# Kernel tuning notes

Hardware: AMD Instinct MI355X
Metric: run time of the kernel (lower is better)

The kernel has to match this reference:

```python
import jax, jax.numpy as jnp
import numpy as np

HIDDEN = 1024
N_HEAD = 16
HEAD_DIM = HIDDEN // N_HEAD


def _rope(x):
    # x: [b, h, l, d]; interleaved RoPE, matching the torch module exactly
    L, d = x.shape[-2], x.shape[-1]
    pos = jnp.arange(L, dtype=x.dtype)[:, None]                      # [L, 1]
    ids = jnp.arange(d // 2, dtype=x.dtype)
    theta = jnp.power(jnp.asarray(10000.0, x.dtype), 2.0 * ids / d)  # [d/2]
    ang = pos / theta                                                # [L, d/2]
    sin = jnp.repeat(jnp.sin(ang), 2, axis=-1)                       # [L, d]
    cos = jnp.repeat(jnp.cos(ang), 2, axis=-1)                       # [L, d]
    # rotate pairs: (x0, x1) -> (-x1, x0)
    x_rot = jnp.stack([-x[..., 1::2], x[..., 0::2]], axis=-1).reshape(x.shape)
    return x * cos + x_rot * sin


def setup_inputs() -> dict:
    key = jax.random.key(0)
    ks = jax.random.split(key, 5)
    B, LQ, LK = 8, 1024, 2048
    scale = 1.0 / np.sqrt(HIDDEN)
    return {
        "x": jax.random.normal(ks[0], (B, LQ, HIDDEN), dtype=jnp.float32),
        "y": jax.random.normal(ks[1], (B, LK, HIDDEN), dtype=jnp.float32),
        "Wq": jax.random.normal(ks[2], (HIDDEN, HIDDEN), dtype=jnp.float32) * scale,
        "Wkv": jax.random.normal(ks[3], (2 * HIDDEN, HIDDEN), dtype=jnp.float32) * scale,
        "Wo": jax.random.normal(ks[4], (HIDDEN, HIDDEN), dtype=jnp.float32) * scale,
    }


def reference(x, y, Wq, Wkv, Wo):
    B, LQ, _ = x.shape
    LK = y.shape[1]
    # projections (torch Linear: out = in @ W.T)
    q = (x @ Wq.T).reshape(B, LQ, N_HEAD, HEAD_DIM).transpose(0, 2, 1, 3)   # [b,h,lq,d]
    kv = (y @ Wkv.T).reshape(B, LK, N_HEAD, 2 * HEAD_DIM).transpose(0, 2, 1, 3)
    k, v = jnp.split(kv, 2, axis=-1)                                         # [b,h,lk,d] each
    q = _rope(q)
    k = _rope(k)
    # NOTE: the original forward does NOT apply self.scale, no dropout, no mask (eval mode)
    scores = jnp.einsum("bhqd,bhkd->bhqk", q, k)
    probs = jax.nn.softmax(scores, axis=-1)
    out = jnp.einsum("bhqk,bhkd->bhqd", probs, v)
    out = out.transpose(0, 2, 1, 3).reshape(B, LQ, HIDDEN)
    return out @ Wo.T
```

## Files before the change

kernel.cpp:

```cpp
#include <hip/hip_runtime.h>

typedef _Float16 f16;
typedef __attribute__((ext_vector_type(8))) _Float16 f16x8;
typedef __attribute__((ext_vector_type(4))) _Float16 f16x4;
typedef __attribute__((ext_vector_type(2))) _Float16 f16x2;
typedef __attribute__((ext_vector_type(4))) float f32x4;

constexpr int B_ = 8, LQ = 1024, LK = 2048, NH = 16, HID = 1024;

__device__ __forceinline__ void gll16(const void* g, void* l) {
  __builtin_amdgcn_global_load_lds((const __attribute__((address_space(1))) void*)g,
                                   (__attribute__((address_space(3))) void*)l, 16, 0, 0);
}

__device__ __forceinline__ f16x2 cvt_pk(float a, float b) {
  return __builtin_bit_cast(f16x2, __builtin_amdgcn_cvt_pkrtz(a, b));
}

constexpr int NQ0 = B_ * LQ * HID / 4;
constexpr int NQ1 = B_ * LK * HID / 4;
constexpr int NQ2 = HID * HID / 4;
constexpr int NQ3 = 2 * HID * HID / 4;
constexpr int NQ4 = HID * HID / 4;
constexpr int NQT = NQ0 + NQ1 + NQ2 + NQ3 + NQ4;

__device__ __forceinline__ void cvt4(const float* __restrict__ s, f16* __restrict__ d, int i) {
  float4 v = ((const float4*)s)[i];
  f16x4 o = {(f16)v.x, (f16)v.y, (f16)v.z, (f16)v.w};
  ((f16x4*)d)[i] = o;
}

__global__ __launch_bounds__(256) void cvt5(const float* __restrict__ x,
                                            const float* __restrict__ y,
                                            const float* __restrict__ wq,
                                            const float* __restrict__ wkv,
                                            const float* __restrict__ wo,
                                            f16* __restrict__ xb, f16* __restrict__ yb,
                                            f16* __restrict__ wqb, f16* __restrict__ wkvb,
                                            f16* __restrict__ wob) {
  int t = blockIdx.x * 256 + threadIdx.x;
  if (t < NQ0) cvt4(x, xb, t);
  else if (t < NQ0 + NQ1) cvt4(y, yb, t - NQ0);
  else if (t < NQ0 + NQ1 + NQ2) cvt4(wq, wqb, t - NQ0 - NQ1);
  else if (t < NQ0 + NQ1 + NQ2 + NQ3) cvt4(wkv, wkvb, t - NQ0 - NQ1 - NQ2);
  else cvt4(wo, wob, t - NQ0 - NQ1 - NQ2 - NQ3);
}

template <int MODE>
__global__ __launch_bounds__(256) void gemm_fused(const f16* __restrict__ A,
                                                  const f16* __restrict__ Bm,
                                                  void* __restrict__ out0,
                                                  void* __restrict__ out1,
                                                  int M, int N, int K) {
  const int gx = gridDim.x;
  const int nwg = gx * gridDim.y;
  const int cpx = nwg >> 3;
  const int fid = blockIdx.y * gx + blockIdx.x;
  const int lid = (fid & 7) * cpx + (fid >> 3);
  const int n0 = (lid % gx) * 128, m0 = (lid / gx) * 128;
  const int tid = threadIdx.x, lane = tid & 63, w = tid >> 6;
  const int wm = w >> 1, wn = w & 1;
  const int quad = lane >> 4, l16 = lane & 15;
  __shared__ __align__(16) f16 As[2][128 * 64];
  __shared__ __align__(16) f16 Bs[2][128 * 64];
  f32x4 acc[4][4] = {};
  const int sr = tid >> 3, sc8 = tid & 7;
  const int ldst = sr * 64 + sc8 * 8;
  const f16* ga = A + (size_t)(m0 + sr) * K + ((sc8 ^ (sr & 7)) << 3);
  const f16* gb = Bm + (size_t)(n0 + sr) * K + ((sc8 ^ (sr & 7)) << 3);
  const int NT = K >> 6;

  auto STAGE = [&](int t) {
    f16* as = As[t & 1];
    f16* bs = Bs[t & 1];
    const int k0 = t << 6;
#pragma unroll
    for (int p = 0; p < 4; ++p) {
      gll16(ga + (size_t)p * 32 * K + k0, &as[ldst + p * 32 * 64]);
      gll16(gb + (size_t)p * 32 * K + k0, &bs[ldst + p * 32 * 64]);
    }
  };

  STAGE(0);
  asm volatile("s_waitcnt vmcnt(0)" ::: "memory");
  __builtin_amdgcn_s_barrier();
  __builtin_amdgcn_sched_barrier(0);

  const int swr = l16 & 7;
  for (int t = 0; t < NT; ++t) {
    if (t + 1 < NT) STAGE(t + 1);
    const f16* as = As[t & 1];
    const f16* bs = Bs[t & 1];
#pragma unroll
    for (int ks = 0; ks < 2; ++ks) {
      f16x8 af[4], bfr[4];
#pragma unroll
      for (int i = 0; i < 4; ++i) {
        const int csw = ((ks * 4 + quad) ^ swr) << 3;
        af[i] = *(const f16x8*)&as[(wm * 64 + i * 16 + l16) * 64 + csw];
        bfr[i] = *(const f16x8*)&bs[(wn * 64 + i * 16 + l16) * 64 + csw];
      }
      __builtin_amdgcn_s_setprio(1);
#pragma unroll
      for (int i = 0; i < 4; ++i)
#pragma unroll
        for (int j = 0; j < 4; ++j)
          acc[i][j] = __builtin_amdgcn_mfma_f32_16x16x32_f16(af[i], bfr[j], acc[i][j], 0, 0, 0);
      __builtin_amdgcn_s_setprio(0);
    }
    asm volatile("s_waitcnt vmcnt(0)" ::: "memory");
    __builtin_amdgcn_s_barrier();
    __builtin_amdgcn_sched_barrier(0);
  }
  if (MODE == 2) {
#pragma unroll
    for (int i = 0; i < 4; ++i)
#pragma unroll
      for (int j = 0; j < 4; ++j) {
        int row = m0 + wm * 64 + i * 16 + quad * 4;
        int col = n0 + wn * 64 + j * 16 + l16;
#pragma unroll
        for (int r = 0; r < 4; ++r)
          ((float*)out0)[(size_t)(row + r) * N + col] = acc[i][j][r];
      }
    return;
  }
  constexpr int LSH = (MODE == 0) ? 10 : 11;
  constexpr int LMSK = (MODE == 0) ? 1023 : 2047;
  const int Ltok = LMSK + 1;
  constexpr float QSCALE = (MODE == 0) ? 1.44269504f : 1.0f;
  if (MODE == 0 || wn == 0) {
#pragma unroll
    for (int j = 0; j < 4; ++j) {
      int c = n0 + wn * 64 + j * 16 + l16;
      int h = (MODE == 0) ? (c >> 6) : (n0 >> 7);
      int d = (MODE == 0) ? (c & 63) : (j * 16 + l16);
      float inv_t = exp2f((float)(d >> 1) * -0.41524101186091903f);
#pragma unroll
      for (int i = 0; i < 4; ++i) {
        f32x4 v = acc[i][j];
        f32x4 pv;
#pragma unroll
        for (int r = 0; r < 4; ++r) pv[r] = __shfl_xor(v[r], 1, 64);
        int row0 = m0 + wm * 64 + i * 16 + quad * 4;
#pragma unroll
        for (int r = 0; r < 4; ++r) {
          int row = row0 + r;
          int pos = row & LMSK, b = row >> LSH;
          float ang = (float)pos * inv_t;
          float sn, cs;
          __sincosf(ang, &sn, &cs);
          float o = (d & 1) ? (v[r] * cs + pv[r] * sn) : (v[r] * cs - pv[r] * sn);
          int dsw = (MODE == 1) ? (d ^ ((pos & 7) << 3)) : d;
          ((f16*)out0)[(((size_t)b * NH + h) * Ltok + pos) * 64 + dsw] = (f16)(o * QSCALE);
        }
      }
    }
  } else {
    const int h = n0 >> 7;
#pragma unroll
    for (int j = 0; j < 4; ++j) {
      int dv = j * 16 + l16;
#pragma unroll
      for (int i = 0; i < 4; ++i) {
        int row0 = m0 + wm * 64 + i * 16 + quad * 4;
        int pos0 = row0 & 2047, b = row0 >> 11;
        int kc = pos0 >> 6, klo = pos0 & 63;
        f32x4 v = acc[i][j];
        f16x4 pk = {(f16)v[0], (f16)v[1], (f16)v[2], (f16)v[3]};
        int klosw = klo ^ ((dv & 7) << 3);
        *(f16x4*)&((f16*)out1)[((((size_t)b * NH + h) * 32 + kc) * 64 + dv) * 64 + klosw] = pk;
      }
    }
  }
}

__global__ __launch_bounds__(256, 4) void attn(const f16* __restrict__ Qb,
                                               const f16* __restrict__ Kb,
                                               const f16* __restrict__ Vt,
                                               f16* __restrict__ attnb) {
  const int fid = blockIdx.x;
  const int lid = (fid & 7) * 128 + (fid >> 3);
  const int bh = lid >> 3, b = bh >> 4, h = bh & 15;
  const int q0 = (lid & 7) * 128;
  const int tid = threadIdx.x, lane = tid & 63, w = tid >> 6;
  const int quad = lane >> 4, l16 = lane & 15;
  const int sw = (l16 & 7) << 3;
  __shared__ __align__(16) f16 Ks[2][64 * 64];
  __shared__ __align__(16) f16 Vts[2][64 * 64];
  const f16* qptr = Qb + ((size_t)bh * LQ + q0 + 32 * w + l16) * 64;
  f16x8 qf[2][2];
#pragma unroll
  for (int qs = 0; qs < 2; ++qs) {
    qf[qs][0] = *(const f16x8*)&qptr[qs * 16 * 64 + quad * 8];
    qf[qs][1] = *(const f16x8*)&qptr[qs * 16 * 64 + 32 + quad * 8];
  }
  const f16x4 ones4 = {(f16)1.f, (f16)1.f, (f16)1.f, (f16)1.f};
  f32x4 o[2][4] = {};
  f32x4 lacc[2] = {};
  float m_run[2] = {0.0f, 0.0f};
  const f16* kbase = Kb + (size_t)bh * LK * 64;
  const f16* vtb = Vt + (size_t)bh * 32 * 4096;
  const int sr = tid >> 3, sc = (tid & 7) * 8;

  auto STAGE = [&](int c) {
    f16* ks = Ks[c & 1];
    f16* vs = Vts[c & 1];
    gll16(kbase + (size_t)(c * 64 + sr) * 64 + sc, &ks[sr * 64 + sc]);
    gll16(kbase + (size_t)(c * 64 + sr + 32) * 64 + sc, &ks[(sr + 32) * 64 + sc]);
    gll16(vtb + (size_t)(c * 64 + sr) * 64 + sc, &vs[sr * 64 + sc]);
    gll16(vtb + (size_t)(c * 64 + sr + 32) * 64 + sc, &vs[(sr + 32) * 64 + sc]);
  };

  constexpr int NC = LK / 64;
  STAGE(0);
  asm volatile("s_waitcnt vmcnt(0)" ::: "memory");
  __builtin_amdgcn_s_barrier();
  __builtin_amdgcn_sched_barrier(0);

  for (int c = 0; c < NC; ++c) {
    if (c + 1 < NC) STAGE(c + 1);
    const f16* Ksb = Ks[c & 1];
    const f16* Vsb = Vts[c & 1];
    f32x4 minit[2];
#pragma unroll
    for (int qs = 0; qs < 2; ++qs)
#pragma unroll
      for (int r = 0; r < 4; ++r) minit[qs][r] = -m_run[qs];
    f32x4 sacc[2][4];
#pragma unroll
    for (int nt = 0; nt < 4; ++nt) {
      const f16* krow = &Ksb[(nt * 16 + l16) * 64];
      f16x8 kf0 = *(const f16x8*)&krow[(quad * 8) ^ sw];
      f16x8 kf1 = *(const f16x8*)&krow[(32 + quad * 8) ^ sw];
      __builtin_amdgcn_s_setprio(1);
#pragma unroll
      for (int qs = 0; qs < 2; ++qs) {
        sacc[qs][nt] = __builtin_amdgcn_mfma_f32_16x16x32_f16(kf0, qf[qs][0], minit[qs], 0, 0, 0);
        sacc[qs][nt] = __builtin_amdgcn_mfma_f32_16x16x32_f16(kf1, qf[qs][1], sacc[qs][nt], 0, 0, 0);
      }
      __builtin_amdgcn_s_setprio(0);
    }
#pragma unroll
    for (int qs = 0; qs < 2; ++qs) {
      f32x4 mm;
#pragma unroll
      for (int r = 0; r < 4; ++r)
        mm[r] = fmaxf(fmaxf(sacc[qs][0][r], sacc[qs][1][r]),
                      fmaxf(sacc[qs][2][r], sacc[qs][3][r]));
      float mx = fmaxf(fmaxf(mm[0], mm[1]), fmaxf(mm[2], mm[3]));
      mx = fmaxf(mx, __shfl_xor(mx, 16, 64));
      mx = fmaxf(mx, __shfl_xor(mx, 32, 64));
      if (!__all(mx <= 11.5415603f)) {
        float dm = fmaxf(mx, 0.0f);
        float al = __builtin_amdgcn_exp2f(-dm);
        m_run[qs] += dm;
#pragma unroll
        for (int r = 0; r < 4; ++r) lacc[qs][r] *= al;
#pragma unroll
        for (int dt = 0; dt < 4; ++dt)
#pragma unroll
          for (int r = 0; r < 4; ++r) o[qs][dt][r] *= al;
#pragma unroll
        for (int nt = 0; nt < 4; ++nt)
#pragma unroll
          for (int r = 0; r < 4; ++r) sacc[qs][nt][r] -= dm;
      }
    }
#pragma unroll
    for (int nt = 0; nt < 4; ++nt) {
      f16x4 vv[4];
#pragma unroll
      for (int dt = 0; dt < 4; ++dt)
        vv[dt] = *(const f16x4*)&Vsb[(dt * 16 + l16) * 64 + ((nt * 16 + quad * 4) ^ sw)];
      f16x4 pq[2];
#pragma unroll
      for (int qs = 0; qs < 2; ++qs) {
        float e0 = __builtin_amdgcn_exp2f(sacc[qs][nt][0]);
        float e1 = __builtin_amdgcn_exp2f(sacc[qs][nt][1]);
        float e2 = __builtin_amdgcn_exp2f(sacc[qs][nt][2]);
        float e3 = __builtin_amdgcn_exp2f(sacc[qs][nt][3]);
        f16x2 lo = cvt_pk(e0, e1);
        f16x2 hi = cvt_pk(e2, e3);
        f16x4 p;
        p[0] = lo[0]; p[1] = lo[1]; p[2] = hi[0]; p[3] = hi[1];
        pq[qs] = p;
      }
      __builtin_amdgcn_s_setprio(1);
#pragma unroll
      for (int qs = 0; qs < 2; ++qs) {
        lacc[qs] = __builtin_amdgcn_mfma_f32_16x16x16f16(ones4, pq[qs], lacc[qs], 0, 0, 0);
#pragma unroll
        for (int dt = 0; dt < 4; ++dt)
          o[qs][dt] = __builtin_amdgcn_mfma_f32_16x16x16f16(vv[dt], pq[qs], o[qs][dt], 0, 0, 0);
      }
      __builtin_amdgcn_s_setprio(0);
    }
    asm volatile("s_waitcnt vmcnt(0)" ::: "memory");
    __builtin_amdgcn_s_barrier();
    __builtin_amdgcn_sched_barrier(0);
  }
#pragma unroll
  for (int qs = 0; qs < 2; ++qs) {
    float inv = 1.0f / lacc[qs][0];
    int q = q0 + 32 * w + qs * 16 + l16;
#pragma unroll
    for (int dt = 0; dt < 4; ++dt) {
      f16x4 ov;
#pragma unroll
      for (int r = 0; r < 4; ++r) ov[r] = (f16)(o[qs][dt][r] * inv);
      *(f16x4*)&attnb[((size_t)b * LQ + q) * HID + h * 64 + dt * 16 + quad * 4] = ov;
    }
  }
}

extern "C" void kernel_launch(void* const* d_in, const int* in_sizes, int n_in,
                              void* d_out, int out_size, void* d_ws, size_t ws_size,
                              hipStream_t stream) {
  const float* x = (const float*)d_in[0];
  const float* y = (const float*)d_in[1];
  const float* Wq = (const float*)d_in[2];
  const float* Wkv = (const float*)d_in[3];
  const float* Wo = (const float*)d_in[4];
  float* out = (float*)d_out;

  char* p = (char*)d_ws;
  f16* xb = (f16*)p;    p += (size_t)B_ * LQ * HID * 2;
  f16* yb = (f16*)p;    p += (size_t)B_ * LK * HID * 2;
  f16* Wqb = (f16*)p;   p += (size_t)HID * HID * 2;
  f16* Wkvb = (f16*)p;  p += (size_t)2 * HID * HID * 2;
  f16* Wob = (f16*)p;   p += (size_t)HID * HID * 2;
  f16* Qb = (f16*)p;    p += (size_t)B_ * LQ * HID * 2;
  f16* Kb = (f16*)p;    p += (size_t)B_ * LK * HID * 2;
  f16* Vt = (f16*)p;    p += (size_t)B_ * LK * HID * 2;
  f16* attnb = xb;

  cvt5<<<dim3(NQT / 256), 256, 0, stream>>>(x, y, Wq, Wkv, Wo, xb, yb, Wqb, Wkvb, Wob);

  gemm_fused<0><<<dim3(HID / 128, B_ * LQ / 128), 256, 0, stream>>>(
      xb, Wqb, Qb, nullptr, B_ * LQ, HID, HID);
  gemm_fused<1><<<dim3(2 * HID / 128, B_ * LK / 128), 256, 0, stream>>>(
      yb, Wkvb, Kb, Vt, B_ * LK, 2 * HID, HID);

  attn<<<dim3(B_ * NH * (LQ / 128)), 256, 0, stream>>>(Qb, Kb, Vt, attnb);

  gemm_fused<2><<<dim3(HID / 128, B_ * LQ / 128), 256, 0, stream>>>(
      attnb, Wob, out, nullptr, B_ * LQ, HID, HID);
}
```

Measured before the change: 384.4 us.

## Merge Q and KV projection GEMMs into one launch and stagger attention KV chunk order

Combines the Q projection and KV projection GEMMs into a single grid of 2560 workgroups, with block-id swizzling that picks the source matrices and the epilogue per tile. This removes one kernel launch and the tail of the smaller Q GEMM. In the attention kernel, different query-block groups start their KV chunk loop at rotated offsets, so concurrent workgroups read different K/V addresses, which is meant to reduce cache and channel contention. The online softmax does not depend on chunk order, so results should hold apart from rounding, and branching on the tile type adds some divergence in the epilogue code.

Measured after the change: 393.3 us. +2.3%, slower.

```diff
diff --git a/kernel.cpp b/kernel.cpp
--- a/kernel.cpp
+++ b/kernel.cpp
@@ -46,12 +46,151 @@
   else cvt4(wo, wob, t - NQ0 - NQ1 - NQ2 - NQ3);
 }
 
-template <int MODE>
-__global__ __launch_bounds__(256) void gemm_fused(const f16* __restrict__ A,
-                                                  const f16* __restrict__ Bm,
-                                                  void* __restrict__ out0,
-                                                  void* __restrict__ out1,
-                                                  int M, int N, int K) {
+__global__ __launch_bounds__(256) void gemm01(const f16* __restrict__ xb,
+                                              const f16* __restrict__ Wqb,
+                                              const f16* __restrict__ yb,
+                                              const f16* __restrict__ Wkvb,
+                                              f16* __restrict__ Qb,
+                                              f16* __restrict__ Kb,
+                                              f16* __restrict__ Vt) {
+  constexpr int K = 1024, NT = K >> 6;
+  constexpr int NB1 = 2048, CPX = 2560 >> 3;
+  const int fid = blockIdx.x;
+  const int lid = (fid & 7) * CPX + (fid >> 3);
+  const bool isQ = lid >= NB1;
+  const int sl = isQ ? (lid - NB1) : lid;
+  const int gx = isQ ? 8 : 16;
+  const int n0 = (sl % gx) * 128, m0 = (sl / gx) * 128;
+  const f16* A = isQ ? xb : yb;
+  const f16* Bm = isQ ? Wqb : Wkvb;
+  const int tid = threadIdx.x, lane = tid & 63, w = tid >> 6;
+  const int wm = w >> 1, wn = w & 1;
+  const int quad = lane >> 4, l16 = lane & 15;
+  __shared__ __align__(16) f16 As[2][128 * 64];
+  __shared__ __align__(16) f16 Bs[2][128 * 64];
+  f32x4 acc[4][4] = {};
+  const int sr = tid >> 3, sc8 = tid & 7;
+  const int ldst = sr * 64 + sc8 * 8;
+  const f16* ga = A + (size_t)(m0 + sr) * K + ((sc8 ^ (sr & 7)) << 3);
+  const f16* gb = Bm + (size_t)(n0 + sr) * K + ((sc8 ^ (sr & 7)) << 3);
+
+  auto STAGE = [&](int t) {
+    f16* as = As[t & 1];
+    f16* bs = Bs[t & 1];
+    const int k0 = t << 6;
+#pragma unroll
+    for (int p = 0; p < 4; ++p) {
+      gll16(ga + (size_t)p * 32 * K + k0, &as[ldst + p * 32 * 64]);
+      gll16(gb + (size_t)p * 32 * K + k0, &bs[ldst + p * 32 * 64]);
+    }
+  };
+
+  STAGE(0);
+  asm volatile("s_waitcnt vmcnt(0)" ::: "memory");
+  __builtin_amdgcn_s_barrier();
+  __builtin_amdgcn_sched_barrier(0);
+
+  const int swr = l16 & 7;
+  for (int t = 0; t < NT; ++t) {
+    if (t + 1 < NT) STAGE(t + 1);
+    const f16* as = As[t & 1];
+    const f16* bs = Bs[t & 1];
+#pragma unroll
+    for (int ks = 0; ks < 2; ++ks) {
+      f16x8 af[4], bfr[4];
+#pragma unroll
+      for (int i = 0; i < 4; ++i) {
+        const int csw = ((ks * 4 + quad) ^ swr) << 3;
+        af[i] = *(const f16x8*)&as[(wm * 64 + i * 16 + l16) * 64 + csw];
+        bfr[i] = *(const f16x8*)&bs[(wn * 64 + i * 16 + l16) * 64 + csw];
+      }
+      __builtin_amdgcn_s_setprio(1);
+#pragma unroll
+      for (int i = 0; i < 4; ++i)
+#pragma unroll
+        for (int j = 0; j < 4; ++j)
+          acc[i][j] = __builtin_amdgcn_mfma_f32_16x16x32_f16(af[i], bfr[j], acc[i][j], 0, 0, 0);
+      __builtin_amdgcn_s_setprio(0);
+    }
+    asm volatile("s_waitcnt vmcnt(0)" ::: "memory");
+    __builtin_amdgcn_s_barrier();
+    __builtin_amdgcn_sched_barrier(0);
+  }
+
+  if (isQ) {
+#pragma unroll
+    for (int j = 0; j < 4; ++j) {
+      int c = n0 + wn * 64 + j * 16 + l16;
+      int h = c >> 6, d = c & 63;
+      float inv_t = exp2f((float)(d >> 1) * -0.41524101186091903f);
+#pragma unroll
+      for (int i = 0; i < 4; ++i) {
+        f32x4 v = acc[i][j];
+        f32x4 pv;
+#pragma unroll
+        for (int r = 0; r < 4; ++r) pv[r] = __shfl_xor(v[r], 1, 64);
+        int row0 = m0 + wm * 64 + i * 16 + quad * 4;
+#pragma unroll
+        for (int r = 0; r < 4; ++r) {
+          int row = row0 + r;
+          int pos = row & 1023, b = row >> 10;
+          float ang = (float)pos * inv_t;
+          float sn, cs;
+          __sincosf(ang, &sn, &cs);
+          float o = (d & 1) ? (v[r] * cs + pv[r] * sn) : (v[r] * cs - pv[r] * sn);
+          Qb[(((size_t)b * NH + h) * LQ + pos) * 64 + d] = (f16)(o * 1.44269504f);
+        }
+      }
+    }
+  } else if (wn == 0) {
+    const int h = n0 >> 7;
+#pragma unroll
+    for (int j = 0; j < 4; ++j) {
+      int d = j * 16 + l16;
+      float inv_t = exp2f((float)(d >> 1) * -0.41524101186091903f);
+#pragma unroll
+      for (int i = 0; i < 4; ++i) {
+        f32x4 v = acc[i][j];
+        f32x4 pv;
+#pragma unroll
+        for (int r = 0; r < 4; ++r) pv[r] = __shfl_xor(v[r], 1, 64);
+        int row0 = m0 + wm * 64 + i * 16 + quad * 4;
+#pragma unroll
+        for (int r = 0; r < 4; ++r) {
+          int row = row0 + r;
+          int pos = row & 2047, b = row >> 11;
+          float ang = (float)pos * inv_t;
+          float sn, cs;
+          __sincosf(ang, &sn, &cs);
+          float o = (d & 1) ? (v[r] * cs + pv[r] * sn) : (v[r] * cs - pv[r] * sn);
+          int dsw = d ^ ((pos & 7) << 3);
+          Kb[(((size_t)b * NH + h) * LK + pos) * 64 + dsw] = (f16)o;
+        }
+      }
+    }
+  } else {
+    const int h = n0 >> 7;
+#pragma unroll
+    for (int j = 0; j < 4; ++j) {
+      int dv = j * 16 + l16;
+#pragma unroll
+      for (int i = 0; i < 4; ++i) {
+        int row0 = m0 + wm * 64 + i * 16 + quad * 4;
+        int pos0 = row0 & 2047, b = row0 >> 11;
+        int kc = pos0 >> 6, klo = pos0 & 63;
+        f32x4 v = acc[i][j];
+        f16x4 pk = {(f16)v[0], (f16)v[1], (f16)v[2], (f16)v[3]};
+        int klosw = klo ^ ((dv & 7) << 3);
+        *(f16x4*)&Vt[((((size_t)b * NH + h) * 32 + kc) * 64 + dv) * 64 + klosw] = pk;
+      }
+    }
+  }
+}
+
+__global__ __launch_bounds__(256) void gemm2(const f16* __restrict__ A,
+                                             const f16* __restrict__ Bm,
+                                             float* __restrict__ out0,
+                                             int M, int N, int K) {
   const int gx = gridDim.x;
   const int nwg = gx * gridDim.y;
   const int cpx = nwg >> 3;
@@ -112,67 +251,16 @@
     __builtin_amdgcn_s_barrier();
     __builtin_amdgcn_sched_barrier(0);
   }
-  if (MODE == 2) {
-#pragma unroll
-    for (int i = 0; i < 4; ++i)
-#pragma unroll
-      for (int j = 0; j < 4; ++j) {
-        int row = m0 + wm * 64 + i * 16 + quad * 4;
-        int col = n0 + wn * 64 + j * 16 + l16;
-#pragma unroll
-        for (int r = 0; r < 4; ++r)
-          ((float*)out0)[(size_t)(row + r) * N + col] = acc[i][j][r];
-      }
-    return;
-  }
-  constexpr int LSH = (MODE == 0) ? 10 : 11;
-  constexpr int LMSK = (MODE == 0) ? 1023 : 2047;
-  const int Ltok = LMSK + 1;
-  constexpr float QSCALE = (MODE == 0) ? 1.44269504f : 1.0f;
-  if (MODE == 0 || wn == 0) {
+#pragma unroll
+  for (int i = 0; i < 4; ++i)
 #pragma unroll
     for (int j = 0; j < 4; ++j) {
-      int c = n0 + wn * 64 + j * 16 + l16;
-      int h = (MODE == 0) ? (c >> 6) : (n0 >> 7);
-      int d = (MODE == 0) ? (c & 63) : (j * 16 + l16);
-      float inv_t = exp2f((float)(d >> 1) * -0.41524101186091903f);
-#pragma unroll
-      for (int i = 0; i < 4; ++i) {
-        f32x4 v = acc[i][j];
-        f32x4 pv;
-#pragma unroll
-        for (int r = 0; r < 4; ++r) pv[r] = __shfl_xor(v[r], 1, 64);
-        int row0 = m0 + wm * 64 + i * 16 + quad * 4;
-#pragma unroll
-        for (int r = 0; r < 4; ++r) {
-          int row = row0 + r;
-          int pos = row & LMSK, b = row >> LSH;
-          float ang = (float)pos * inv_t;
-          float sn, cs;
-          __sincosf(ang, &sn, &cs);
-          float o = (d & 1) ? (v[r] * cs + pv[r] * sn) : (v[r] * cs - pv[r] * sn);
-          int dsw = (MODE == 1) ? (d ^ ((pos & 7) << 3)) : d;
-          ((f16*)out0)[(((size_t)b * NH + h) * Ltok + pos) * 64 + dsw] = (f16)(o * QSCALE);
-        }
-      }
-    }
-  } else {
-    const int h = n0 >> 7;
-#pragma unroll
-    for (int j = 0; j < 4; ++j) {
-      int dv = j * 16 + l16;
-#pragma unroll
-      for (int i = 0; i < 4; ++i) {
-        int row0 = m0 + wm * 64 + i * 16 + quad * 4;
-        int pos0 = row0 & 2047, b = row0 >> 11;
-        int kc = pos0 >> 6, klo = pos0 & 63;
-        f32x4 v = acc[i][j];
-        f16x4 pk = {(f16)v[0], (f16)v[1], (f16)v[2], (f16)v[3]};
-        int klosw = klo ^ ((dv & 7) << 3);
-        *(f16x4*)&((f16*)out1)[((((size_t)b * NH + h) * 32 + kc) * 64 + dv) * 64 + klosw] = pk;
-      }
-    }
-  }
+      int row = m0 + wm * 64 + i * 16 + quad * 4;
+      int col = n0 + wn * 64 + j * 16 + l16;
+#pragma unroll
+      for (int r = 0; r < 4; ++r)
+        out0[(size_t)(row + r) * N + col] = acc[i][j][r];
+    }
 }
 
 __global__ __launch_bounds__(256, 4) void attn(const f16* __restrict__ Qb,
@@ -183,6 +271,7 @@
   const int lid = (fid & 7) * 128 + (fid >> 3);
   const int bh = lid >> 3, b = bh >> 4, h = bh & 15;
   const int q0 = (lid & 7) * 128;
+  const int off = ((lid >> 5) & 3) << 3;
   const int tid = threadIdx.x, lane = tid & 63, w = tid >> 6;
   const int quad = lane >> 4, l16 = lane & 15;
   const int sw = (l16 & 7) << 3;
@@ -204,12 +293,13 @@
   const int sr = tid >> 3, sc = (tid & 7) * 8;
 
   auto STAGE = [&](int c) {
+    const int cc = (c + off) & 31;
     f16* ks = Ks[c & 1];
     f16* vs = Vts[c & 1];
-    gll16(kbase + (size_t)(c * 64 + sr) * 64 + sc, &ks[sr * 64 + sc]);
-    gll16(kbase + (size_t)(c * 64 + sr + 32) * 64 + sc, &ks[(sr + 32) * 64 + sc]);
-    gll16(vtb + (size_t)(c * 64 + sr) * 64 + sc, &vs[sr * 64 + sc]);
-    gll16(vtb + (size_t)(c * 64 + sr + 32) * 64 + sc, &vs[(sr + 32) * 64 + sc]);
+    gll16(kbase + (size_t)(cc * 64 + sr) * 64 + sc, &ks[sr * 64 + sc]);
+    gll16(kbase + (size_t)(cc * 64 + sr + 32) * 64 + sc, &ks[(sr + 32) * 64 + sc]);
+    gll16(vtb + (size_t)(cc * 64 + sr) * 64 + sc, &vs[sr * 64 + sc]);
+    gll16(vtb + (size_t)(cc * 64 + sr + 32) * 64 + sc, &vs[(sr + 32) * 64 + sc]);
   };
 
   constexpr int NC = LK / 64;
@@ -337,13 +427,10 @@
 
   cvt5<<<dim3(NQT / 256), 256, 0, stream>>>(x, y, Wq, Wkv, Wo, xb, yb, Wqb, Wkvb, Wob);
 
-  gemm_fused<0><<<dim3(HID / 128, B_ * LQ / 128), 256, 0, stream>>>(
-      xb, Wqb, Qb, nullptr, B_ * LQ, HID, HID);
-  gemm_fused<1><<<dim3(2 * HID / 128, B_ * LK / 128), 256, 0, stream>>>(
-      yb, Wkvb, Kb, Vt, B_ * LK, 2 * HID, HID);
+  gemm01<<<dim3(2560), 256, 0, stream>>>(xb, Wqb, yb, Wkvb, Qb, Kb, Vt);
 
   attn<<<dim3(B_ * NH * (LQ / 128)), 256, 0, stream>>>(Qb, Kb, Vt, attnb);
 
-  gemm_fused<2><<<dim3(HID / 128, B_ * LQ / 128), 256, 0, stream>>>(
-      attnb, Wob, out, nullptr, B_ * LQ, HID, HID);
-}
+  gemm2<<<dim3(HID / 128, B_ * LQ / 128), 256, 0, stream>>>(
+      attnb, Wob, out, B_ * LQ, HID, HID);
+}
```
